# Performance work log

Hardware: AMD Instinct MI355X
Metric: run time of the kernel (lower is better)

Reference implementation:

```python
import jax, jax.numpy as jnp
import numpy as np

L_GNN = 4          # num_layers - 1
NUM_GRAPHS = 64
BN_EPS = 1e-5


def _bn(x, g, b):
    # torch BatchNorm1d in training mode: biased variance, per-feature affine
    m = x.mean(axis=0)
    v = ((x - m) ** 2).mean(axis=0)
    return g * (x - m) * jax.lax.rsqrt(v + BN_EPS) + b


def _mlp(x, W1, b1, g, bb, W2, b2):
    # GIN 2-layer MLP: Linear -> BN -> ReLU -> Linear
    h = jax.nn.relu(_bn(x @ W1 + b1, g, bb))
    return h @ W2 + b2


def setup_inputs():
    key = jax.random.key(0)
    ks = jax.random.split(key, 20)
    N1, N2, E1, E2 = 8192, 4096, 262144, 65536
    D1, D2, H, O = 128, 64, 512, 10

    def nrm(k, shape, scale=0.05):
        return (jax.random.normal(k, shape) * scale).astype(jnp.float32)

    return {
        "x1": jax.random.normal(ks[0], (N1, D1), jnp.float32),
        "x2": jax.random.normal(ks[1], (N2, D2), jnp.float32),
        "motif2A": jax.random.uniform(ks[2], (N2, N1), jnp.float32),
        "edge1": jax.random.randint(ks[3], (2, E1), 0, N1),
        "edge2": jax.random.randint(ks[4], (2, E2), 0, N2),
        "graph_ids": jnp.sort(jax.random.randint(ks[5], (N1,), 0, NUM_GRAPHS)),
        "eps": jnp.zeros((L_GNN,), jnp.float32),
        "atts": jax.random.uniform(ks[6], (2,), jnp.float32),
        "mlp1_W1_0": nrm(ks[7], (D1, H)),
        "mlp1_W1_rest": nrm(ks[8], (L_GNN - 1, 2 * H, H)),
        "mlp1_b1": jnp.zeros((L_GNN, H), jnp.float32),
        "mlp1_bn_g": jnp.ones((L_GNN, H), jnp.float32),
        "mlp1_bn_b": jnp.zeros((L_GNN, H), jnp.float32),
        "mlp1_W2": nrm(ks[9], (L_GNN, H, H)),
        "mlp1_b2": jnp.zeros((L_GNN, H), jnp.float32),
        "bn1_g": jnp.ones((L_GNN, H), jnp.float32),
        "bn1_b": jnp.zeros((L_GNN, H), jnp.float32),
        "mlp2_W1_0": nrm(ks[10], (D2, H)),
        "mlp2_W1_rest": nrm(ks[11], (L_GNN - 1, H, H)),
        "mlp2_b1": jnp.zeros((L_GNN, H), jnp.float32),
        "mlp2_bn_g": jnp.ones((L_GNN, H), jnp.float32),
        "mlp2_bn_b": jnp.zeros((L_GNN, H), jnp.float32),
        "mlp2_W2": nrm(ks[12], (L_GNN, H, H)),
        "mlp2_b2": jnp.zeros((L_GNN, H), jnp.float32),
        "bn2_g": jnp.ones((L_GNN, H), jnp.float32),
        "bn2_b": jnp.zeros((L_GNN, H), jnp.float32),
        "pred_W0": nrm(ks[13], (D1, O)),
        "pred_b0": jnp.zeros((O,), jnp.float32),
        "pred_W": nrm(ks[14], (L_GNN, 2 * H, O)),
        "pred_b": jnp.zeros((L_GNN, O), jnp.float32),
    }


def reference(x1, x2, motif2A, edge1, edge2, graph_ids, eps, atts,
              mlp1_W1_0, mlp1_W1_rest, mlp1_b1, mlp1_bn_g, mlp1_bn_b, mlp1_W2, mlp1_b2,
              bn1_g, bn1_b,
              mlp2_W1_0, mlp2_W1_rest, mlp2_b1, mlp2_bn_g, mlp2_bn_b, mlp2_W2, mlp2_b2,
              bn2_g, bn2_b,
              pred_W0, pred_b0, pred_W, pred_b):
    N1, N2 = x1.shape[0], x2.shape[0]
    a = jax.nn.softmax(atts)                      # attention over [self-graph, hyper-graph]
    h1, h2 = x1, x2
    hidden = [x1]
    for l in range(L_GNN):
        # spmm(Adj, h) == scatter-sum of source features onto destination rows
        pooled1 = jax.ops.segment_sum(h1[edge1[1]], edge1[0], num_segments=N1)
        pooled1 = pooled1 + (1.0 + eps[l]) * h1   # learn_eps branch (next_layer_eps)
        W1 = mlp1_W1_0 if l == 0 else mlp1_W1_rest[l - 1]
        rep1 = _mlp(pooled1, W1, mlp1_b1[l], mlp1_bn_g[l], mlp1_bn_b[l], mlp1_W2[l], mlp1_b2[l])
        h1 = jax.nn.relu(_bn(rep1, bn1_g[l], bn1_b[l]))
        # hyper graph branch
        pooled2 = jax.ops.segment_sum(h2[edge2[1]], edge2[0], num_segments=N2)
        pooled2 = pooled2 + (1.0 + eps[l]) * h2
        W1h = mlp2_W1_0 if l == 0 else mlp2_W1_rest[l - 1]
        rep2 = _mlp(pooled2, W1h, mlp2_b1[l], mlp2_bn_g[l], mlp2_bn_b[l], mlp2_W2[l], mlp2_b2[l])
        h2 = jax.nn.relu(_bn(rep2, bn2_g[l], bn2_b[l]))
        # project hyper-node features back to base nodes and fuse with attention
        h2A = motif2A.T @ h2                      # [N1, H]
        h1 = jnp.concatenate([a[0] * h1, a[1] * h2A], axis=1)  # [N1, 2H]
        hidden.append(h1)
    # jumping-knowledge readout: sum graph pooling + per-layer linear heads
    score = jax.ops.segment_sum(hidden[0], graph_ids, num_segments=NUM_GRAPHS) @ pred_W0 + pred_b0
    for l in range(L_GNN):
        pooled_h = jax.ops.segment_sum(hidden[l + 1], graph_ids, num_segments=NUM_GRAPHS)
        score = score + pooled_h @ pred_W[l] + pred_b[l]
    return score
```

## Files before the change

### kernel.cpp

```cpp
#include <hip/hip_runtime.h>

using bf16x8 = __attribute__((ext_vector_type(8))) short;
using f32x4  = __attribute__((ext_vector_type(4))) float;
using u16x4  = __attribute__((ext_vector_type(4))) unsigned short;
using u16x8  = __attribute__((ext_vector_type(8))) unsigned short;
using as3_void  = __attribute__((address_space(3))) void;
using as1_cvoid = const __attribute__((address_space(1))) void;

__device__ __forceinline__ unsigned short f2bf(float x) {
    union { float f; unsigned u; } v; v.f = x;
    unsigned r = v.u + 0x7FFFu + ((v.u >> 16) & 1u);
    return (unsigned short)(r >> 16);
}
__device__ __forceinline__ float bf2f(unsigned short h) {
    union { unsigned u; float f; } v; v.u = ((unsigned)h) << 16;
    return v.f;
}

#define GEMM_BODY(BM, A, Bt, K, KBEG, KEND)                                          \
    constexpr int WROWS = (BM) / 2;                                                  \
    constexpr int MI = WROWS / 16;                                                   \
    __shared__ __align__(16) unsigned short As[(BM) * 64];                           \
    __shared__ __align__(16) unsigned short Bs[128 * 64];                            \
    const int tid  = threadIdx.x;                                                    \
    const int lane = tid & 63, wave = tid >> 6;                                      \
    const int wr = wave >> 1, wc = wave & 1;                                         \
    const int rl = lane & 15, kg = lane >> 4;                                        \
    f32x4 acc[MI][4] = {};                                                           \
    for (int kt = (KBEG); kt < (KEND); kt += 64) {                                   \
        _Pragma("unroll")                                                            \
        for (int it = 0; it < (BM) / 32; ++it) {                                     \
            int slot = it * 256 + tid;                                               \
            int r = slot >> 3, c = slot & 7;                                         \
            int cg = c ^ (r & 7);                                                    \
            const unsigned short* ga = (A) + (size_t)(m0 + r) * (K) + (kt + cg * 8); \
            __builtin_amdgcn_global_load_lds((as1_cvoid*)ga, (as3_void*)(As + slot * 8), 16, 0, 0); \
        }                                                                            \
        _Pragma("unroll")                                                            \
        for (int it = 0; it < 4; ++it) {                                             \
            int slot = it * 256 + tid;                                               \
            int r = slot >> 3, c = slot & 7;                                         \
            int cg = c ^ (r & 7);                                                    \
            const unsigned short* gb = (Bt) + (size_t)(n0 + r) * (K) + (kt + cg * 8);\
            __builtin_amdgcn_global_load_lds((as1_cvoid*)gb, (as3_void*)(Bs + slot * 8), 16, 0, 0); \
        }                                                                            \
        __syncthreads();                                                             \
        _Pragma("unroll")                                                            \
        for (int kh = 0; kh < 2; ++kh) {                                             \
            bf16x8 a_[MI], b_[4];                                                    \
            _Pragma("unroll")                                                        \
            for (int i = 0; i < MI; ++i) {                                           \
                int ra = wr * WROWS + i * 16 + rl;                                   \
                int ca = (kh * 4 + kg) ^ (ra & 7);                                   \
                a_[i] = *reinterpret_cast<const bf16x8*>(&As[ra * 64 + ca * 8]);     \
            }                                                                        \
            _Pragma("unroll")                                                        \
            for (int j = 0; j < 4; ++j) {                                            \
                int rb = wc * 64 + j * 16 + rl;                                      \
                int cb = (kh * 4 + kg) ^ (rb & 7);                                   \
                b_[j] = *reinterpret_cast<const bf16x8*>(&Bs[rb * 64 + cb * 8]);     \
            }                                                                        \
            _Pragma("unroll")                                                        \
            for (int i = 0; i < MI; ++i)                                             \
                _Pragma("unroll")                                                    \
                for (int j = 0; j < 4; ++j)                                          \
                    acc[i][j] = __builtin_amdgcn_mfma_f32_16x16x32_bf16(a_[i], b_[j], acc[i][j], 0, 0, 0); \
        }                                                                            \
        __syncthreads();                                                             \
    }

__global__ __launch_bounds__(256) void gemm_dual(
    int nb0,
    const unsigned short* __restrict__ A0, const unsigned short* __restrict__ B0,
    int K0, unsigned short* __restrict__ C0, float* __restrict__ st0,
    const unsigned short* __restrict__ A1, const unsigned short* __restrict__ B1,
    int K1, unsigned short* __restrict__ C1, float* __restrict__ st1)
{
    int bx = blockIdx.x;
    const unsigned short *A, *Bt; unsigned short* Cb; float* statp;
    int K;
    if (bx < nb0) { A = A0; Bt = B0; K = K0; Cb = C0; statp = st0; }
    else { bx -= nb0; A = A1; Bt = B1; K = K1; Cb = C1; statp = st1; }
    const int m0 = bx * 64, n0 = blockIdx.y * 128;

    GEMM_BODY(64, A, Bt, K, 0, K)

#pragma unroll
    for (int i = 0; i < MI; ++i)
#pragma unroll
        for (int j = 0; j < 4; ++j)
#pragma unroll
            for (int e = 0; e < 4; ++e) {
                int rr = m0 + wr * WROWS + i * 16 + kg * 4 + e;
                int cc = n0 + wc * 64 + j * 16 + rl;
                Cb[(size_t)rr * 512 + cc] = f2bf(acc[i][j][e]);
            }
    if (statp) {
#pragma unroll
        for (int j = 0; j < 4; ++j) {
            float s = 0.f, q = 0.f;
#pragma unroll
            for (int i = 0; i < MI; ++i)
#pragma unroll
                for (int e = 0; e < 4; ++e) {
                    float x = acc[i][j][e];
                    s += x; q += x * x;
                }
            s += __shfl_xor(s, 16); s += __shfl_xor(s, 32);
            q += __shfl_xor(q, 16); q += __shfl_xor(q, 32);
            if (kg == 0) {
                int cc = n0 + wc * 64 + j * 16 + rl;
                atomicAdd(&statp[cc], s);
                atomicAdd(&statp[512 + cc], q);
            }
        }
    }
}

__global__ __launch_bounds__(256) void gemm_splitk(
    const unsigned short* __restrict__ A, const unsigned short* __restrict__ Bt,
    int M, int N, int K, float* __restrict__ Cp)
{
    const int m0 = blockIdx.x * 128, n0 = blockIdx.y * 128;
    const int kn = K / gridDim.z, kbeg = blockIdx.z * kn;

    GEMM_BODY(128, A, Bt, K, kbeg, kbeg + kn)

    float* dst = Cp + (size_t)blockIdx.z * M * N;
#pragma unroll
    for (int i = 0; i < MI; ++i)
#pragma unroll
        for (int j = 0; j < 4; ++j)
#pragma unroll
            for (int e = 0; e < 4; ++e) {
                int rr = m0 + wr * WROWS + i * 16 + kg * 4 + e;
                int cc = n0 + wc * 64 + j * 16 + rl;
                dst[(size_t)rr * N + cc] = acc[i][j][e];
            }
}

__global__ void csr_count2(const int* __restrict__ e1, int E1, int* __restrict__ c1,
                           const int* __restrict__ e2, int E2, int* __restrict__ c2) {
    int i = blockIdx.x * 256 + threadIdx.x;
    if (i < E1) atomicAdd(&c1[e1[i]], 1);
    else if (i < E1 + E2) atomicAdd(&c2[e2[i - E1]], 1);
}

__global__ void csr_scan2(const int* __restrict__ cnt1, int n1, int* __restrict__ offs1, int* __restrict__ cur1,
                          const int* __restrict__ cnt2, int n2, int* __restrict__ offs2, int* __restrict__ cur2) {
    const int* cnt = blockIdx.x ? cnt2 : cnt1;
    int n           = blockIdx.x ? n2 : n1;
    int* offs       = blockIdx.x ? offs2 : offs1;
    int* cursor     = blockIdx.x ? cur2 : cur1;
    __shared__ int part[1024];
    int t = threadIdx.x;
    int per = n >> 10;
    int base = t * per;
    int loc[8];
    int s = 0;
    for (int j = 0; j < per; ++j) { loc[j] = s; s += cnt[base + j]; }
    part[t] = s;
    __syncthreads();
    for (int o = 1; o < 1024; o <<= 1) {
        int v = (t >= o) ? part[t - o] : 0;
        __syncthreads();
        part[t] += v;
        __syncthreads();
    }
    int excl = (t == 0) ? 0 : part[t - 1];
    for (int j = 0; j < per; ++j) {
        int v = excl + loc[j];
        offs[base + j] = v;
        cursor[base + j] = v;
    }
    if (t == 1023) offs[n] = part[1023];
}

__global__ void csr_fill2(const int* __restrict__ e1, int E1, int* __restrict__ cur1, int* __restrict__ s1,
                          const int* __restrict__ e2, int E2, int* __restrict__ cur2, int* __restrict__ s2) {
    int i = blockIdx.x * 256 + threadIdx.x;
    if (i < E1) {
        int d = e1[i], s = e1[E1 + i];
        s1[atomicAdd(&cur1[d], 1)] = s;
    } else if (i < E1 + E2) {
        int e = i - E1;
        int d = e2[e], s = e2[E2 + e];
        s2[atomicAdd(&cur2[d], 1)] = s;
    }
}

__global__ __launch_bounds__(128) void gather2_bf16(
    const u16x4* __restrict__ Y1, const int* __restrict__ offs1, const int* __restrict__ srcs1,
    u16x4* __restrict__ T1, int n1,
    const u16x4* __restrict__ Y2, const int* __restrict__ offs2, const int* __restrict__ srcs2,
    u16x4* __restrict__ T2,
    const float* __restrict__ epsv, int l)
{
    int i = blockIdx.x;
    const u16x4* Y; u16x4* T; const int *offs, *srcs;
    if (i < n1) { Y = Y1; T = T1; offs = offs1; srcs = srcs1; }
    else        { i -= n1; Y = Y2; T = T2; offs = offs2; srcs = srcs2; }
    int c = threadIdx.x;
    float e = 1.0f + epsv[l];
    int lo = offs[i], hi = offs[i + 1];
    u16x4 hv = Y[(size_t)i * 128 + c];
    f32x4 a0, a1 = {}, a2 = {}, a3 = {};
#pragma unroll
    for (int j = 0; j < 4; ++j) a0[j] = e * bf2f(hv[j]);
    int k = lo;
    for (; k + 4 <= hi; k += 4) {
        int s0 = srcs[k], s1 = srcs[k + 1], s2 = srcs[k + 2], s3 = srcs[k + 3];
        u16x4 v0 = Y[(size_t)s0 * 128 + c];
        u16x4 v1 = Y[(size_t)s1 * 128 + c];
        u16x4 v2 = Y[(size_t)s2 * 128 + c];
        u16x4 v3 = Y[(size_t)s3 * 128 + c];
#pragma unroll
        for (int j = 0; j < 4; ++j) {
            a0[j] += bf2f(v0[j]); a1[j] += bf2f(v1[j]);
            a2[j] += bf2f(v2[j]); a3[j] += bf2f(v3[j]);
        }
    }
    for (; k < hi; ++k) {
        u16x4 v = Y[(size_t)srcs[k] * 128 + c];
#pragma unroll
        for (int j = 0; j < 4; ++j) a0[j] += bf2f(v[j]);
    }
    f32x4 acc = (a0 + a1) + (a2 + a3);
    u16x4 o;
#pragma unroll
    for (int j = 0; j < 4; ++j) o[j] = f2bf(acc[j]);
    T[(size_t)i * 128 + c] = o;
}

__global__ void bn_stats2(int nb0,
                          const u16x4* __restrict__ X0, float* __restrict__ ss0,
                          const u16x4* __restrict__ X1, float* __restrict__ ss1) {
    int bx = blockIdx.x;
    const u16x4* X; float* ss;
    if (bx < nb0) { X = X0; ss = ss0; }
    else { bx -= nb0; X = X1; ss = ss1; }
    int c = threadIdx.x;
    int r0 = bx * 16;
    f32x4 s = {}, q = {};
    for (int r = 0; r < 16; ++r) {
        u16x4 v = X[(size_t)(r0 + r) * 128 + c];
        f32x4 f;
#pragma unroll
        for (int j = 0; j < 4; ++j) f[j] = bf2f(v[j]);
        s += f; q += f * f;
    }
#pragma unroll
    for (int j = 0; j < 4; ++j) {
        atomicAdd(&ss[c * 4 + j], s[j]);
        atomicAdd(&ss[512 + c * 4 + j], q[j]);
    }
}

__global__ __launch_bounds__(128) void bn_apply_mid(
    int nb0,
    const u16x4* __restrict__ X0, int M0, const float* __restrict__ ss0,
    const float* __restrict__ g0, const float* __restrict__ b0, unsigned short* __restrict__ o0,
    const u16x4* __restrict__ X1, int M1, const float* __restrict__ ss1,
    const float* __restrict__ g1, const float* __restrict__ b1, unsigned short* __restrict__ o1)
{
    int bx = blockIdx.x;
    const u16x4* X; const float *ss, *g, *b; unsigned short* out; int M;
    if (bx < nb0) { X = X0; M = M0; ss = ss0; g = g0; b = b0; out = o0; }
    else { bx -= nb0; X = X1; M = M1; ss = ss1; g = g1; b = b1; out = o1; }
    int c = threadIdx.x;
    float inv = 1.0f / (float)M;
    float al[4], be[4];
#pragma unroll
    for (int i = 0; i < 4; ++i) {
        float mean = ss[c * 4 + i] * inv;
        float var  = ss[512 + c * 4 + i] * inv - mean * mean;
        al[i] = g[c * 4 + i] * rsqrtf(var + 1e-5f);
        be[i] = b[c * 4 + i] - mean * al[i];
    }
    int r0 = bx * 8;
    for (int r = 0; r < 8; ++r) {
        u16x4 v = X[(size_t)(r0 + r) * 128 + c];
        u16x4 h;
#pragma unroll
        for (int i = 0; i < 4; ++i)
            h[i] = f2bf(fmaxf(al[i] * bf2f(v[i]) + be[i], 0.f));
        *reinterpret_cast<u16x4*>(out + (size_t)(r0 + r) * 512 + c * 4) = h;
    }
}

__global__ __launch_bounds__(128) void bn_apply_b2t(
    const u16x4* __restrict__ X, int M, const float* __restrict__ ss,
    const float* __restrict__ g, const float* __restrict__ b,
    unsigned short* __restrict__ out, unsigned short* __restrict__ outT)
{
    int c = threadIdx.x;
    float inv = 1.0f / (float)M;
    float al[4], be[4];
#pragma unroll
    for (int i = 0; i < 4; ++i) {
        float mean = ss[c * 4 + i] * inv;
        float var  = ss[512 + c * 4 + i] * inv - mean * mean;
        al[i] = g[c * 4 + i] * rsqrtf(var + 1e-5f);
        be[i] = b[c * 4 + i] - mean * al[i];
    }
    int r0 = blockIdx.x * 8;
    u16x8 t8[4];
#pragma unroll
    for (int r = 0; r < 8; ++r) {
        u16x4 v = X[(size_t)(r0 + r) * 128 + c];
        u16x4 h;
#pragma unroll
        for (int i = 0; i < 4; ++i) {
            h[i] = f2bf(fmaxf(al[i] * bf2f(v[i]) + be[i], 0.f));
            t8[i][r] = h[i];
        }
        *reinterpret_cast<u16x4*>(out + (size_t)(r0 + r) * 512 + c * 4) = h;
    }
#pragma unroll
    for (int i = 0; i < 4; ++i)
        *reinterpret_cast<u16x8*>(outT + (size_t)(c * 4 + i) * 4096 + r0) = t8[i];
}

__global__ __launch_bounds__(128) void finale(
    int nb0, const int* __restrict__ gid, const float* __restrict__ aDev,
    float* __restrict__ pool, unsigned short* __restrict__ H1,
    const u16x4* __restrict__ X, const float* __restrict__ ss,
    const float* __restrict__ g, const float* __restrict__ b,
    const f32x4* __restrict__ P, int ks)
{
    int bx = blockIdx.x;
    int c = threadIdx.x;
    int job = bx >= nb0;
    if (job) bx -= nb0;
    int r0 = bx * 8;
    int ooff = job ? 512 : 0;
    float al[4], be[4];
    float sc;
    if (!job) {
        sc = aDev[0];
        float inv = 1.0f / 8192.0f;
#pragma unroll
        for (int i = 0; i < 4; ++i) {
            float mean = ss[c * 4 + i] * inv;
            float var  = ss[512 + c * 4 + i] * inv - mean * mean;
            al[i] = g[c * 4 + i] * rsqrtf(var + 1e-5f);
            be[i] = b[c * 4 + i] - mean * al[i];
        }
    } else {
        sc = aDev[1];
    }
    const int total4 = 8192 * 128;
    int curg = gid[r0];
    f32x4 pacc = {};
    for (int r = 0; r < 8; ++r) {
        int row = r0 + r;
        u16x4 h;
        f32x4 f;
        if (!job) {
            u16x4 v = X[(size_t)row * 128 + c];
#pragma unroll
            for (int i = 0; i < 4; ++i) {
                h[i] = f2bf(fmaxf(al[i] * bf2f(v[i]) + be[i], 0.f) * sc);
                f[i] = bf2f(h[i]);
            }
        } else {
            f32x4 s = P[(size_t)row * 128 + c];
            for (int z = 1; z < ks; ++z) s += P[(size_t)z * total4 + (size_t)row * 128 + c];
#pragma unroll
            for (int i = 0; i < 4; ++i) { h[i] = f2bf(s[i] * sc); f[i] = bf2f(h[i]); }
        }
        *reinterpret_cast<u16x4*>(H1 + (size_t)row * 1024 + ooff + c * 4) = h;
        int gg = gid[row];
        if (gg != curg) {
#pragma unroll
            for (int j = 0; j < 4; ++j)
                atomicAdd(&pool[(size_t)curg * 1024 + ooff + c * 4 + j], pacc[j]);
            pacc = {}; curg = gg;
        }
        pacc += f;
    }
#pragma unroll
    for (int j = 0; j < 4; ++j)
        atomicAdd(&pool[(size_t)curg * 1024 + ooff + c * 4 + j], pacc[j]);
}

__global__ void cvt2_bf16(const f32x4* __restrict__ X0, u16x4* __restrict__ O0, int n0,
                          const f32x4* __restrict__ X1, u16x4* __restrict__ O1, int n1) {
    for (int i = blockIdx.x * blockDim.x + threadIdx.x; i < n0 + n1; i += gridDim.x * blockDim.x) {
        const f32x4* X; u16x4* O; int k;
        if (i < n0) { X = X0; O = O0; k = i; }
        else { X = X1; O = O1; k = i - n0; }
        f32x4 v = X[k];
        u16x4 h;
#pragma unroll
        for (int j = 0; j < 4; ++j) h[j] = f2bf(v[j]);
        O[k] = h;
    }
}

__global__ __launch_bounds__(256) void motif_transpose(const float* __restrict__ S,
                                                       unsigned short* __restrict__ D) {
    __shared__ unsigned short tile[64][66];
    int m0 = blockIdx.x * 64;
    int k0 = blockIdx.y * 64;
    int t = threadIdx.x;
    int r = t >> 4, cq = t & 15;
#pragma unroll
    for (int p = 0; p < 4; ++p) {
        int row = r + p * 16;
        f32x4 v = *reinterpret_cast<const f32x4*>(S + (size_t)(k0 + row) * 8192 + m0 + cq * 4);
        u16x4 h;
#pragma unroll
        for (int j = 0; j < 4; ++j) h[j] = f2bf(v[j]);
        *reinterpret_cast<u16x4*>(&tile[row][cq * 4]) = h;
    }
    __syncthreads();
#pragma unroll
    for (int p = 0; p < 4; ++p) {
        int col = r + p * 16;
        u16x4 h;
#pragma unroll
        for (int i = 0; i < 4; ++i) h[i] = tile[cq * 4 + i][col];
        *reinterpret_cast<u16x4*>(D + (size_t)(m0 + col) * 4096 + k0 + cq * 4) = h;
    }
}

__global__ void transpose_cvt_b(const float* __restrict__ S, unsigned short* __restrict__ D,
                                int rows, int cols, size_t sstride, size_t dstride) {
    S += blockIdx.z * sstride; D += blockIdx.z * dstride;
    __shared__ unsigned short tile[32][33];
    int x0 = blockIdx.x * 32, y0 = blockIdx.y * 32;
    for (int j = threadIdx.y; j < 32; j += blockDim.y)
        tile[j][threadIdx.x] = f2bf(S[(size_t)(y0 + j) * cols + x0 + threadIdx.x]);
    __syncthreads();
    for (int j = threadIdx.y; j < 32; j += blockDim.y)
        D[(size_t)(x0 + j) * rows + y0 + threadIdx.x] = tile[threadIdx.x][j];
}

__global__ void transpose_cvt11(const float* __restrict__ A, unsigned short* __restrict__ Ad,
                                const float* __restrict__ B, unsigned short* __restrict__ Bd,
                                const float* __restrict__ Cs, unsigned short* __restrict__ Cd) {
    int z = blockIdx.z;
    const float* S; unsigned short* D;
    if (z < 4)      { S = A  + (size_t)z * 262144;       D = Ad + (size_t)z * 262144; }
    else if (z < 7) { S = B  + (size_t)(z - 4) * 262144; D = Bd + (size_t)(z - 4) * 262144; }
    else            { S = Cs + (size_t)(z - 7) * 262144; D = Cd + (size_t)(z - 7) * 262144; }
    __shared__ unsigned short tile[32][33];
    int x0 = blockIdx.x * 32, y0 = blockIdx.y * 32;
    for (int j = threadIdx.y; j < 32; j += blockDim.y)
        tile[j][threadIdx.x] = f2bf(S[(size_t)(y0 + j) * 512 + x0 + threadIdx.x]);
    __syncthreads();
    for (int j = threadIdx.y; j < 32; j += blockDim.y)
        D[(size_t)(x0 + j) * 512 + y0 + threadIdx.x] = tile[threadIdx.x][j];
}

__device__ __forceinline__ int lbound(const int* __restrict__ a, int n, int v) {
    int lo = 0, hi = n;
    while (lo < hi) { int m = (lo + hi) >> 1; if (a[m] < v) lo = m + 1; else hi = m; }
    return lo;
}

__global__ void pool_f32_at(const float* __restrict__ Hm, const int* __restrict__ gid,
                            int n, float* __restrict__ P) {
    int g = blockIdx.x;
    int lo = lbound(gid, n, g), hi = lbound(gid, n, g + 1);
    int cnt = hi - lo;
    int per = (cnt + 3) >> 2;
    int s = lo + blockIdx.y * per;
    int e = min(s + per, hi);
    if (s >= e) return;
    int c = threadIdx.x;
    f32x4 acc = {};
    for (int i = s; i < e; ++i)
        acc += *reinterpret_cast<const f32x4*>(Hm + (size_t)i * 128 + c * 4);
#pragma unroll
    for (int j = 0; j < 4; ++j)
        atomicAdd(&P[(size_t)g * 128 + c * 4 + j], acc[j]);
}

__global__ void softmax2(const float* __restrict__ atts, float* __restrict__ a) {
    if (threadIdx.x == 0) {
        float m = fmaxf(atts[0], atts[1]);
        float e0 = expf(atts[0] - m), e1 = expf(atts[1] - m);
        float inv = 1.0f / (e0 + e1);
        a[0] = e0 * inv; a[1] = e1 * inv;
    }
}

__global__ __launch_bounds__(256) void score_kernel(
    const float* __restrict__ P0, const float* __restrict__ PL,
    const float* __restrict__ W0, const float* __restrict__ b0,
    const float* __restrict__ W, const float* __restrict__ bb,
    float* __restrict__ out)
{
    int g = blockIdx.x;
    int t = threadIdx.x;
    float part[10];
#pragma unroll
    for (int o = 0; o < 10; ++o) part[o] = 0.f;
    if (t < 128) {
        float p = P0[g * 128 + t];
#pragma unroll
        for (int o = 0; o < 10; ++o) part[o] += p * W0[t * 10 + o];
    }
    for (int l = 0; l < 4; ++l) {
        const float* p = PL + (size_t)l * 65536 + (size_t)g * 1024;
        const float* w = W + (size_t)l * 10240;
        for (int k = t; k < 1024; k += 256) {
            float pv = p[k];
#pragma unroll
            for (int o = 0; o < 10; ++o) part[o] += pv * w[k * 10 + o];
        }
    }
    __shared__ float red[4][10];
#pragma unroll
    for (int o = 0; o < 10; ++o) {
        float v = part[o];
        for (int off = 32; off; off >>= 1) v += __shfl_down(v, off, 64);
        if ((t & 63) == 0) red[t >> 6][o] = v;
    }
    __syncthreads();
    if (t < 10) {
        float s = b0[t] + red[0][t] + red[1][t] + red[2][t] + red[3][t];
#pragma unroll
        for (int l = 0; l < 4; ++l) s += bb[l * 10 + t];
        out[g * 10 + t] = s;
    }
}

extern "C" void kernel_launch(void* const* d_in, const int* in_sizes, int n_in,
                              void* d_out, int out_size, void* d_ws, size_t ws_size,
                              hipStream_t stream) {
    const float* x1    = (const float*)d_in[0];
    const float* x2    = (const float*)d_in[1];
    const float* motif = (const float*)d_in[2];
    const int*   edge1 = (const int*)d_in[3];
    const int*   edge2 = (const int*)d_in[4];
    const int*   gid   = (const int*)d_in[5];
    const float* epsv  = (const float*)d_in[6];
    const float* atts  = (const float*)d_in[7];
    const float* m1W10 = (const float*)d_in[8];
    const float* m1W1r = (const float*)d_in[9];
    const float* m1bng = (const float*)d_in[11];
    const float* m1bnb = (const float*)d_in[12];
    const float* m1W2  = (const float*)d_in[13];
    const float* bn1g  = (const float*)d_in[15];
    const float* bn1b  = (const float*)d_in[16];
    const float* m2W10 = (const float*)d_in[17];
    const float* m2W1r = (const float*)d_in[18];
    const float* m2bng = (const float*)d_in[20];
    const float* m2bnb = (const float*)d_in[21];
    const float* m2W2  = (const float*)d_in[22];
    const float* bn2g  = (const float*)d_in[24];
    const float* bn2b  = (const float*)d_in[25];
    const float* pW0   = (const float*)d_in[26];
    const float* pb0   = (const float*)d_in[27];
    const float* pW    = (const float*)d_in[28];
    const float* pb    = (const float*)d_in[29];
    float* out = (float*)d_out;

    constexpr int N1 = 8192, N2 = 4096, E1 = 262144, E2 = 65536;

    char* base = (char*)d_ws;
    size_t off = 0;
    auto alloc = [&](size_t bytes) -> void* {
        void* p = base + off;
        off = (off + bytes + 255) & ~(size_t)255;
        return p;
    };

    unsigned short* motifT  = (unsigned short*)alloc((size_t)8192 * 4096 * 2);
    unsigned short* w1t1_0  = (unsigned short*)alloc((size_t)512 * 128 * 2);
    unsigned short* w1t1_r  = (unsigned short*)alloc((size_t)3 * 512 * 1024 * 2);
    unsigned short* w2t1    = (unsigned short*)alloc((size_t)4 * 512 * 512 * 2);
    unsigned short* w1t2_0  = (unsigned short*)alloc((size_t)512 * 64 * 2);
    unsigned short* w1t2_r  = (unsigned short*)alloc((size_t)3 * 512 * 512 * 2);
    unsigned short* w2t2    = (unsigned short*)alloc((size_t)4 * 512 * 512 * 2);
    unsigned short* x1b     = (unsigned short*)alloc((size_t)N1 * 128 * 2);
    unsigned short* x2b     = (unsigned short*)alloc((size_t)N2 * 64 * 2);
    unsigned short* H1b     = (unsigned short*)alloc((size_t)N1 * 1024 * 2);
    unsigned short* H2b     = (unsigned short*)alloc((size_t)N2 * 512 * 2);
    unsigned short* H2t     = (unsigned short*)alloc((size_t)512 * 4096 * 2);
    unsigned short* U1b     = (unsigned short*)alloc((size_t)N1 * 512 * 2);
    unsigned short* U2b     = (unsigned short*)alloc((size_t)N2 * 512 * 2);
    unsigned short* Y1b     = (unsigned short*)alloc((size_t)N1 * 512 * 2);
    unsigned short* T1b     = (unsigned short*)alloc((size_t)N1 * 512 * 2);
    unsigned short* Y2b     = (unsigned short*)alloc((size_t)N2 * 512 * 2);
    unsigned short* T2b     = (unsigned short*)alloc((size_t)N2 * 512 * 2);
    int*   cnt1 = (int*)alloc((size_t)N1 * 4);
    int*   cnt2 = (int*)alloc((size_t)N2 * 4);
    float* ss   = (float*)alloc((size_t)16 * 1024 * 4);
    float* PL   = (float*)alloc((size_t)4 * 64 * 1024 * 4);
    float* P0   = (float*)alloc((size_t)64 * 128 * 4);
    const size_t zero_bytes = (size_t)N1 * 4 + N2 * 4 + 16 * 1024 * 4 + 4 * 64 * 1024 * 4
                            + 64 * 128 * 4;
    int*   offs1 = (int*)alloc((size_t)(N1 + 1) * 4);
    int*   offs2 = (int*)alloc((size_t)(N2 + 1) * 4);
    int*   cur1  = (int*)alloc((size_t)N1 * 4);
    int*   cur2  = (int*)alloc((size_t)N2 * 4);
    int*   srcs1 = (int*)alloc((size_t)E1 * 4);
    int*   srcs2 = (int*)alloc((size_t)E2 * 4);
    float* aDev  = (float*)alloc(256);

    if (off > ws_size) return;

    const size_t part_elems = (size_t)N1 * 512;
    size_t rem = ws_size - off;
    int KS = (rem >= 4 * part_elems * 4) ? 4 : (rem >= 2 * part_elems * 4) ? 2 : 1;
    float* Cpart = (float*)(base + off);

    hipMemsetAsync(cnt1, 0, zero_bytes, stream);
    softmax2<<<1, 64, 0, stream>>>(atts, aDev);
    cvt2_bf16<<<512, 256, 0, stream>>>((const f32x4*)x1, (u16x4*)x1b, N1 * 128 / 4,
                                       (const f32x4*)x2, (u16x4*)x2b, N2 * 64 / 4);
    motif_transpose<<<dim3(128, 64), 256, 0, stream>>>(motif, motifT);
    transpose_cvt_b<<<dim3(16, 4, 1), dim3(32, 8), 0, stream>>>(m1W10, w1t1_0, 128, 512, 0, 0);
    transpose_cvt_b<<<dim3(16, 32, 3), dim3(32, 8), 0, stream>>>(m1W1r, w1t1_r, 1024, 512,
                                                                 (size_t)1024 * 512, (size_t)512 * 1024);
    transpose_cvt_b<<<dim3(16, 2, 1), dim3(32, 8), 0, stream>>>(m2W10, w1t2_0, 64, 512, 0, 0);
    transpose_cvt11<<<dim3(16, 16, 11), dim3(32, 8), 0, stream>>>(m1W2, w2t1, m2W1r, w1t2_r, m2W2, w2t2);
    csr_count2<<<(E1 + E2) / 256, 256, 0, stream>>>(edge1, E1, cnt1, edge2, E2, cnt2);
    csr_scan2<<<2, 1024, 0, stream>>>(cnt1, N1, offs1, cur1, cnt2, N2, offs2, cur2);
    csr_fill2<<<(E1 + E2) / 256, 256, 0, stream>>>(edge1, E1, cur1, srcs1, edge2, E2, cur2, srcs2);
    pool_f32_at<<<dim3(64, 4), 32, 0, stream>>>(x1, gid, N1, P0);

    for (int l = 0; l < 4; ++l) {
        float* ssl = ss + (size_t)l * 4096;
        float* PLl = PL + (size_t)l * 65536;
        gemm_dual<<<dim3(192, 4), 256, 0, stream>>>(
            128,
            l ? H1b : x1b, l ? w1t1_r + (size_t)(l - 1) * 512 * 1024 : w1t1_0,
            l ? 1024 : 128, Y1b, nullptr,
            l ? H2b : x2b, l ? w1t2_r + (size_t)(l - 1) * 512 * 512 : w1t2_0,
            l ? 512 : 64, Y2b, nullptr);
        gather2_bf16<<<N1 + N2, 128, 0, stream>>>(
            (const u16x4*)Y1b, offs1, srcs1, (u16x4*)T1b, N1,
            (const u16x4*)Y2b, offs2, srcs2, (u16x4*)T2b, epsv, l);
        bn_stats2<<<768, 128, 0, stream>>>(512, (const u16x4*)T1b, ssl + 0 * 1024,
                                           (const u16x4*)T2b, ssl + 2 * 1024);
        bn_apply_mid<<<1536, 128, 0, stream>>>(
            1024,
            (const u16x4*)T1b, N1, ssl + 0 * 1024, m1bng + l * 512, m1bnb + l * 512, U1b,
            (const u16x4*)T2b, N2, ssl + 2 * 1024, m2bng + l * 512, m2bnb + l * 512, U2b);
        gemm_dual<<<dim3(192, 4), 256, 0, stream>>>(
            128,
            U1b, w2t1 + (size_t)l * 512 * 512, 512, Y1b, ssl + 1 * 1024,
            U2b, w2t2 + (size_t)l * 512 * 512, 512, Y2b, ssl + 3 * 1024);
        bn_apply_b2t<<<512, 128, 0, stream>>>(
            (const u16x4*)Y2b, N2, ssl + 3 * 1024, bn2g + l * 512, bn2b + l * 512, H2b, H2t);
        gemm_splitk<<<dim3(64, 4, KS), 256, 0, stream>>>(motifT, H2t, N1, 512, 4096, Cpart);
        finale<<<2048, 128, 0, stream>>>(
            1024, gid, aDev, PLl, H1b,
            (const u16x4*)Y1b, ssl + 1 * 1024, bn1g + l * 512, bn1b + l * 512,
            (const f32x4*)Cpart, KS);
    }

    score_kernel<<<64, 256, 0, stream>>>(P0, PL, pW0, pb0, pW, pb, out);
}
```

Baseline: 992.0 us.

## Aggregate before first linear layer and swizzle GEMM blocks across XCDs

For layer 0, the neighbour sum is applied to the narrow raw input features before the first MLP weight, using linearity. The GEMM then writes directly into the pre-BN buffer and accumulates BN statistics in its epilogue, so the separate stats pass is dropped and the gather reads much narrower rows. Both GEMM kernels also remap block indices so neighbouring tiles land on the same XCD, to improve L2 reuse. The remap assumes a grid y-dimension of 4 and a block count divisible by 8. BN statistics now come from fp32 accumulators rather than bf16-rounded values.

```diff
diff --git a/kernel.cpp b/kernel.cpp
--- a/kernel.cpp
+++ b/kernel.cpp
@@ -15,6 +15,14 @@
 __device__ __forceinline__ float bf2f(unsigned short h) {
     union { unsigned u; float f; } v; v.u = ((unsigned)h) << 16;
     return v.f;
+}
+
+__device__ __forceinline__ void xcd_remap(int& bx, int& n0) {
+    int flat  = blockIdx.x + gridDim.x * blockIdx.y;
+    int total = gridDim.x * gridDim.y;
+    int swz   = (flat & 7) * (total >> 3) + (flat >> 3);
+    bx = swz >> 2;
+    n0 = (swz & 3) * 128;
 }
 
 #define GEMM_BODY(BM, A, Bt, K, KBEG, KEND)                                          \
@@ -76,12 +84,13 @@
     const unsigned short* __restrict__ A1, const unsigned short* __restrict__ B1,
     int K1, unsigned short* __restrict__ C1, float* __restrict__ st1)
 {
-    int bx = blockIdx.x;
+    int bx, n0;
+    xcd_remap(bx, n0);
     const unsigned short *A, *Bt; unsigned short* Cb; float* statp;
     int K;
     if (bx < nb0) { A = A0; Bt = B0; K = K0; Cb = C0; statp = st0; }
     else { bx -= nb0; A = A1; Bt = B1; K = K1; Cb = C1; statp = st1; }
-    const int m0 = bx * 64, n0 = blockIdx.y * 128;
+    const int m0 = bx * 64;
 
     GEMM_BODY(64, A, Bt, K, 0, K)
 
@@ -121,7 +130,9 @@
     const unsigned short* __restrict__ A, const unsigned short* __restrict__ Bt,
     int M, int N, int K, float* __restrict__ Cp)
 {
-    const int m0 = blockIdx.x * 128, n0 = blockIdx.y * 128;
+    int bx, n0;
+    xcd_remap(bx, n0);
+    const int m0 = bx * 128;
     const int kn = K / gridDim.z, kbeg = blockIdx.z * kn;
 
     GEMM_BODY(128, A, Bt, K, kbeg, kbeg + kn)
@@ -230,6 +241,50 @@
 #pragma unroll
     for (int j = 0; j < 4; ++j) o[j] = f2bf(acc[j]);
     T[(size_t)i * 128 + c] = o;
+}
+
+__global__ __launch_bounds__(64) void gather2_l0(
+    const u16x4* __restrict__ X1, const int* __restrict__ offs1, const int* __restrict__ srcs1,
+    u16x4* __restrict__ T1, int n1,
+    const u16x4* __restrict__ X2, const int* __restrict__ offs2, const int* __restrict__ srcs2,
+    u16x4* __restrict__ T2,
+    const float* __restrict__ epsv)
+{
+    int i = blockIdx.x;
+    const u16x4* X; u16x4* T; const int *offs, *srcs; int nc4;
+    if (i < n1) { X = X1; T = T1; offs = offs1; srcs = srcs1; nc4 = 32; }
+    else        { i -= n1; X = X2; T = T2; offs = offs2; srcs = srcs2; nc4 = 16; }
+    int c = threadIdx.x;
+    if (c >= nc4) return;
+    float e = 1.0f + epsv[0];
+    int lo = offs[i], hi = offs[i + 1];
+    u16x4 hv = X[(size_t)i * nc4 + c];
+    f32x4 a0, a1 = {}, a2 = {}, a3 = {};
+#pragma unroll
+    for (int j = 0; j < 4; ++j) a0[j] = e * bf2f(hv[j]);
+    int k = lo;
+    for (; k + 4 <= hi; k += 4) {
+        int s0 = srcs[k], s1 = srcs[k + 1], s2 = srcs[k + 2], s3 = srcs[k + 3];
+        u16x4 v0 = X[(size_t)s0 * nc4 + c];
+        u16x4 v1 = X[(size_t)s1 * nc4 + c];
+        u16x4 v2 = X[(size_t)s2 * nc4 + c];
+        u16x4 v3 = X[(size_t)s3 * nc4 + c];
+#pragma unroll
+        for (int j = 0; j < 4; ++j) {
+            a0[j] += bf2f(v0[j]); a1[j] += bf2f(v1[j]);
+            a2[j] += bf2f(v2[j]); a3[j] += bf2f(v3[j]);
+        }
+    }
+    for (; k < hi; ++k) {
+        u16x4 v = X[(size_t)srcs[k] * nc4 + c];
+#pragma unroll
+        for (int j = 0; j < 4; ++j) a0[j] += bf2f(v[j]);
+    }
+    f32x4 acc = (a0 + a1) + (a2 + a3);
+    u16x4 o;
+#pragma unroll
+    for (int j = 0; j < 4; ++j) o[j] = f2bf(acc[j]);
+    T[(size_t)i * nc4 + c] = o;
 }
 
 __global__ void bn_stats2(int nb0,
@@ -578,6 +633,8 @@
     unsigned short* w2t2    = (unsigned short*)alloc((size_t)4 * 512 * 512 * 2);
     unsigned short* x1b     = (unsigned short*)alloc((size_t)N1 * 128 * 2);
     unsigned short* x2b     = (unsigned short*)alloc((size_t)N2 * 64 * 2);
+    unsigned short* Tx1     = (unsigned short*)alloc((size_t)N1 * 128 * 2);
+    unsigned short* Tx2     = (unsigned short*)alloc((size_t)N2 * 64 * 2);
     unsigned short* H1b     = (unsigned short*)alloc((size_t)N1 * 1024 * 2);
     unsigned short* H2b     = (unsigned short*)alloc((size_t)N2 * 512 * 2);
     unsigned short* H2t     = (unsigned short*)alloc((size_t)512 * 4096 * 2);
@@ -627,17 +684,25 @@
     for (int l = 0; l < 4; ++l) {
         float* ssl = ss + (size_t)l * 4096;
         float* PLl = PL + (size_t)l * 65536;
-        gemm_dual<<<dim3(192, 4), 256, 0, stream>>>(
-            128,
-            l ? H1b : x1b, l ? w1t1_r + (size_t)(l - 1) * 512 * 1024 : w1t1_0,
-            l ? 1024 : 128, Y1b, nullptr,
-            l ? H2b : x2b, l ? w1t2_r + (size_t)(l - 1) * 512 * 512 : w1t2_0,
-            l ? 512 : 64, Y2b, nullptr);
-        gather2_bf16<<<N1 + N2, 128, 0, stream>>>(
-            (const u16x4*)Y1b, offs1, srcs1, (u16x4*)T1b, N1,
-            (const u16x4*)Y2b, offs2, srcs2, (u16x4*)T2b, epsv, l);
-        bn_stats2<<<768, 128, 0, stream>>>(512, (const u16x4*)T1b, ssl + 0 * 1024,
-                                           (const u16x4*)T2b, ssl + 2 * 1024);
+        if (l == 0) {
+            gather2_l0<<<N1 + N2, 64, 0, stream>>>(
+                (const u16x4*)x1b, offs1, srcs1, (u16x4*)Tx1, N1,
+                (const u16x4*)x2b, offs2, srcs2, (u16x4*)Tx2, epsv);
+            gemm_dual<<<dim3(192, 4), 256, 0, stream>>>(
+                128,
+                Tx1, w1t1_0, 128, T1b, ssl + 0 * 1024,
+                Tx2, w1t2_0, 64,  T2b, ssl + 2 * 1024);
+        } else {
+            gemm_dual<<<dim3(192, 4), 256, 0, stream>>>(
+                128,
+                H1b, w1t1_r + (size_t)(l - 1) * 512 * 1024, 1024, Y1b, nullptr,
+                H2b, w1t2_r + (size_t)(l - 1) * 512 * 512,  512,  Y2b, nullptr);
+            gather2_bf16<<<N1 + N2, 128, 0, stream>>>(
+                (const u16x4*)Y1b, offs1, srcs1, (u16x4*)T1b, N1,
+                (const u16x4*)Y2b, offs2, srcs2, (u16x4*)T2b, epsv, l);
+            bn_stats2<<<768, 128, 0, stream>>>(512, (const u16x4*)T1b, ssl + 0 * 1024,
+                                               (const u16x4*)T2b, ssl + 2 * 1024);
+        }
         bn_apply_mid<<<1536, 128, 0, stream>>>(
             1024,
             (const u16x4*)T1b, N1, ssl + 0 * 1024, m1bng + l * 512, m1bnb + l * 512, U1b,
```

New measurement: 916.4 us. 7.6% less time.
